# Kernel tuning notes

Hardware: AMD Instinct MI355X
Metric: run time of the kernel (lower is better)

Reference implementation:

```python
import jax, jax.numpy as jnp
import numpy as np

B, S = 2, 2048
HQ, HKV, D = 32, 8, 128
SCALING = 0.08838834764831845  # 1/sqrt(128)
E4M3_MAX = 448.0
FP4_MAX = 6.0
# e2m1 representable magnitudes and decision midpoints
FP4_GRID = jnp.array([0.0, 0.5, 1.0, 1.5, 2.0, 3.0, 4.0, 6.0], dtype=jnp.float32)
FP4_MID = (FP4_GRID[:-1] + FP4_GRID[1:]) / 2.0


def quant_dequant_e4m3(x):
    """Simulate torch .to(float8_e4m3fn): clamp to +-448, round mantissa to 3 bits."""
    ax = jnp.abs(x)
    xc = jnp.clip(x, -E4M3_MAX, E4M3_MAX)
    e = jnp.clip(jnp.floor(jnp.log2(jnp.maximum(ax, 1e-12))), -6.0, 8.0)
    q = jnp.round(xc * jnp.exp2(3.0 - e)) * jnp.exp2(e - 3.0)
    return jnp.where(ax == 0.0, 0.0, q)


def quant_dequant_fp4(x):
    """FP4 (e2m1) compress/decompress with per-(token,head) absmax scale over head_dim.
    x: [B, S, H, D] -> dequantized [B, S, H, D]."""
    scale = jnp.max(jnp.abs(x), axis=-1, keepdims=True) / FP4_MAX  # [B,S,H,1]
    scale = jnp.maximum(scale, 1e-12)
    xn = x / scale
    idx = jnp.searchsorted(FP4_MID, jnp.abs(xn))  # nearest e2m1 magnitude
    return jnp.sign(xn) * FP4_GRID[idx] * scale


def setup_inputs() -> dict:
    key = jax.random.key(0)
    kq, kk, kv = jax.random.split(key, 3)
    q = jax.random.normal(kq, (B, S, HQ * D), dtype=jnp.float32)
    k = jax.random.normal(kk, (B, S, HKV * D), dtype=jnp.float32)
    v = jax.random.normal(kv, (B, S, HKV * D), dtype=jnp.float32)
    return {"q": q, "k": k, "v": v}


def reference(q, k, v):
    # reshape to heads
    qh = q.reshape(B, S, HQ, D)
    kh = k.reshape(B, S, HKV, D)
    vh = v.reshape(B, S, HKV, D)
    # FP8 cast then FP4 compress/decompress of the KV cache
    kq8 = quant_dequant_e4m3(kh)
    vq8 = quant_dequant_e4m3(vh)
    kd = quant_dequant_fp4(kq8)
    vd = quant_dequant_fp4(vq8)
    # GQA: expand kv heads to query heads
    g = HQ // HKV
    kr = jnp.repeat(kd, g, axis=2)  # [B,S,HQ,D]
    vr = jnp.repeat(vd, g, axis=2)
    scores = jnp.einsum("bqhd,bkhd->bhqk", qh, kr) * SCALING  # [B,HQ,S,S]
    causal = jnp.tril(jnp.ones((S, S), dtype=bool))
    scores = jnp.where(causal[None, None], scores, jnp.float32(-1e30))
    probs = jax.nn.softmax(scores, axis=-1)
    out = jnp.einsum("bhqk,bkhd->bqhd", probs, vr)
    return out.reshape(B, S, HQ * D)
```

## Files before the change

### kernel.cpp

```cpp
#include <hip/hip_runtime.h>
#include <cstdint>
#include <cstddef>

#define B_    2
#define S_    2048
#define HQ_   32
#define HKV_  8
#define D_    128
#define SCALING_ 0.08838834764831845f

#define NROW_ (B_*S_*HKV_)

typedef __bf16 bf16x8 __attribute__((ext_vector_type(8)));
typedef float  f32x4  __attribute__((ext_vector_type(4)));

__device__ __forceinline__ unsigned short f2bfu(float f) {
    __bf16 b = (__bf16)f;
    return __builtin_bit_cast(unsigned short, b);
}

__device__ __forceinline__ float qd_e4m3(float x) {
    float ax = fabsf(x);
    float xc = fminf(fmaxf(x, -448.f), 448.f);
    int ex;
    (void)frexpf(fmaxf(ax, 1e-12f), &ex);
    int e = ex - 1;
    e = min(max(e, -6), 8);
    float q = rintf(ldexpf(xc, 3 - e));
    q = ldexpf(q, e - 3);
    return ax == 0.f ? 0.f : q;
}

__device__ __forceinline__ float qd_fp4(float x, float scale) {
    float xn = x / scale;
    float a = fabsf(xn);
    float g;
    if      (a <= 0.25f) g = 0.f;
    else if (a <= 0.75f) g = 0.5f;
    else if (a <= 1.25f) g = 1.f;
    else if (a <= 1.75f) g = 1.5f;
    else if (a <= 2.5f)  g = 2.f;
    else if (a <= 3.5f)  g = 3.f;
    else if (a <= 5.f)   g = 4.f;
    else                 g = 6.f;
    return copysignf(g * scale, xn);
}

__global__ __launch_bounds__(256) void quant_kv(const float* __restrict__ k,
                                                const float* __restrict__ v,
                                                unsigned short* __restrict__ kd,
                                                unsigned short* __restrict__ vd) {
    int gw = (blockIdx.x * 256 + threadIdx.x) >> 6;
    int lane = threadIdx.x & 63;
    int row = gw;
    const float* src;
    unsigned short* dst;
    if (row < NROW_) { src = k; dst = kd; }
    else             { row -= NROW_; src = v; dst = vd; }
    int b   = row / (S_ * HKV_);
    int rem = row - b * (S_ * HKV_);
    int s   = rem >> 3;
    int h   = rem & 7;
    float2 x = *(const float2*)(src + (size_t)row * D_ + 2 * lane);
    float q0 = qd_e4m3(x.x);
    float q1 = qd_e4m3(x.y);
    float amax = fmaxf(fabsf(q0), fabsf(q1));
#pragma unroll
    for (int m = 1; m < 64; m <<= 1) amax = fmaxf(amax, __shfl_xor(amax, m, 64));
    float scale = fmaxf(amax / 6.0f, 1e-12f);
    float y0 = qd_fp4(q0, scale);
    float y1 = qd_fp4(q1, scale);
    size_t outOff = ((size_t)(b * HKV_ + h) * S_ + s) * D_ + 2 * lane;
    unsigned int pack = (unsigned int)f2bfu(y0) | ((unsigned int)f2bfu(y1) << 16);
    *(unsigned int*)(dst + outOff) = pack;
}

__global__ __launch_bounds__(256) void transpose_v(const unsigned short* __restrict__ vd,
                                                   unsigned short* __restrict__ vdT) {
    __shared__ alignas(16) unsigned short t[64][136];
    int bh = blockIdx.x >> 5;
    int st = blockIdx.x & 31;
    int s0 = st * 64;
    int tid = threadIdx.x;
    {
        int row = tid >> 2;
        const unsigned short* sp = vd + ((size_t)bh * S_ + s0 + row) * D_;
#pragma unroll
        for (int i = 0; i < 4; ++i) {
            int c = (tid & 3) + 4 * i;
            *(uint4*)&t[row][c * 8] = *(const uint4*)(sp + c * 8);
        }
    }
    __syncthreads();
    {
        int d = tid >> 1;
        unsigned short* dp = vdT + ((size_t)bh * D_ + d) * S_ + s0;
#pragma unroll
        for (int i = 0; i < 4; ++i) {
            int c = (tid & 1) + 2 * i;
            int so = c * 8;
            unsigned short tmp[8];
#pragma unroll
            for (int e = 0; e < 8; ++e) tmp[e] = t[so + e][d];
            *(uint4*)(dp + so) = *(uint4*)tmp;
        }
    }
}

__global__ __launch_bounds__(256) void attn(const float* __restrict__ q,
                                            const unsigned short* __restrict__ kd,
                                            const unsigned short* __restrict__ vdT,
                                            float* __restrict__ out) {
    int bh = blockIdx.x;
    int yp = blockIdx.y;
    int b  = bh >> 5;
    int hq = bh & 31;
    int hkv = hq >> 2;
    int tid  = threadIdx.x;
    int lane = tid & 63;
    int wave = tid >> 6;
    int m16  = lane & 15;
    int g    = lane >> 4;

    __shared__ alignas(16) unsigned short ks[64 * 128];
    __shared__ alignas(16) unsigned short vs[128 * 64];
    __shared__ alignas(16) unsigned short ps[4 * 16 * 64];

    const unsigned short* kbase = kd  + (size_t)(b * HKV_ + hkv) * S_ * D_;
    const unsigned short* vbase = vdT + (size_t)(b * HKV_ + hkv) * D_ * S_;

    bf16x8 vones;
#pragma unroll
    for (int j = 0; j < 8; ++j) vones[j] = (__bf16)1.0f;

    for (int phase = 0; phase < 2; ++phase) {
        int qt = phase ? yp : (31 - yp);
        int q0 = qt * 64;
        int qrowBase = q0 + wave * 16;

        bf16x8 qf[4];
        const float* qp = q + (((size_t)b * S_ + (qrowBase + m16)) * HQ_ + hq) * D_;
#pragma unroll
        for (int c = 0; c < 4; ++c) {
            const float* p0 = qp + c * 32 + g * 8;
            bf16x8 f;
#pragma unroll
            for (int j = 0; j < 8; ++j) f[j] = (__bf16)(p0[j] * SCALING_);
            qf[c] = f;
        }

        f32x4 o[8];
#pragma unroll
        for (int i = 0; i < 8; ++i) o[i] = (f32x4){0.f, 0.f, 0.f, 0.f};
        f32x4 o9 = (f32x4){0.f, 0.f, 0.f, 0.f};
        float mr[4];
#pragma unroll
        for (int r = 0; r < 4; ++r) mr[r] = -1e30f;

        for (int kt = 0; kt <= qt; ++kt) {
            int k0 = kt * 64;
            __syncthreads();
            {
                int row = tid >> 2;
                const unsigned short* sp = kbase + (size_t)(k0 + row) * D_;
#pragma unroll
                for (int i = 0; i < 4; ++i) {
                    int c = (tid & 3) + 4 * i;
                    *(uint4*)&ks[row * 128 + ((c ^ (row & 15)) * 8)] =
                        *(const uint4*)(sp + c * 8);
                }
            }
            {
                int d = tid >> 1;
                const unsigned short* sp = vbase + (size_t)d * S_ + k0;
#pragma unroll
                for (int i = 0; i < 4; ++i) {
                    int c = (tid & 1) + 2 * i;
                    *(uint4*)&vs[d * 64 + ((c ^ (d & 7)) * 8)] =
                        *(const uint4*)(sp + c * 8);
                }
            }
            __syncthreads();

            f32x4 sacc[4];
#pragma unroll
            for (int n = 0; n < 4; ++n) sacc[n] = (f32x4){0.f, 0.f, 0.f, 0.f};
#pragma unroll
            for (int n = 0; n < 4; ++n) {
#pragma unroll
                for (int c = 0; c < 4; ++c) {
                    bf16x8 bk = *(const bf16x8*)&ks[(n * 16 + m16) * 128 +
                                                    (((c * 4 + g) ^ m16) * 8)];
                    sacc[n] = __builtin_amdgcn_mfma_f32_16x16x32_bf16(qf[c], bk, sacc[n], 0, 0, 0);
                }
            }

            bool diag = (kt == qt);
            float pvv[4][4];
            float rm[4];
#pragma unroll
            for (int r = 0; r < 4; ++r) rm[r] = -1e30f;
#pragma unroll
            for (int n = 0; n < 4; ++n) {
#pragma unroll
                for (int r = 0; r < 4; ++r) {
                    float sc = sacc[n][r];
                    if (diag) {
                        int key = k0 + n * 16 + m16;
                        int qr  = qrowBase + g * 4 + r;
                        if (key > qr) sc = -1e30f;
                    }
                    pvv[n][r] = sc;
                    rm[r] = fmaxf(rm[r], sc);
                }
            }
#pragma unroll
            for (int r = 0; r < 4; ++r) {
#pragma unroll
                for (int mk = 1; mk < 16; mk <<= 1)
                    rm[r] = fmaxf(rm[r], __shfl_xor(rm[r], mk, 64));
                float mnew  = fmaxf(mr[r], rm[r]);
                float alpha = __expf(mr[r] - mnew);
                mr[r] = mnew;
#pragma unroll
                for (int n = 0; n < 4; ++n)
                    pvv[n][r] = __expf(pvv[n][r] - mnew);
#pragma unroll
                for (int ds = 0; ds < 8; ++ds) o[ds][r] *= alpha;
                o9[r] *= alpha;
            }

#pragma unroll
            for (int n = 0; n < 4; ++n)
#pragma unroll
                for (int r = 0; r < 4; ++r) {
                    int prow = g * 4 + r;
                    ps[wave * 1024 + prow * 64 +
                       (((n * 2 + (m16 >> 3)) ^ (prow & 7)) * 8) + (m16 & 7)] =
                        f2bfu(pvv[n][r]);
                }
            asm volatile("s_waitcnt lgkmcnt(0)" ::: "memory");

            bf16x8 pa[2];
#pragma unroll
            for (int kc = 0; kc < 2; ++kc)
                pa[kc] = *(const bf16x8*)&ps[wave * 1024 + m16 * 64 +
                                             (((kc * 4 + g) ^ (m16 & 7)) * 8)];
#pragma unroll
            for (int kc = 0; kc < 2; ++kc)
                o9 = __builtin_amdgcn_mfma_f32_16x16x32_bf16(pa[kc], vones, o9, 0, 0, 0);
#pragma unroll
            for (int ds = 0; ds < 8; ++ds) {
#pragma unroll
                for (int kc = 0; kc < 2; ++kc) {
                    bf16x8 vb = *(const bf16x8*)&vs[(ds * 16 + m16) * 64 +
                                                    (((kc * 4 + g) ^ (m16 & 7)) * 8)];
                    o[ds] = __builtin_amdgcn_mfma_f32_16x16x32_bf16(pa[kc], vb, o[ds], 0, 0, 0);
                }
            }
        }

#pragma unroll
        for (int r = 0; r < 4; ++r) {
            float inv = 1.f / o9[r];
            float* op = out + (((size_t)b * S_ + (qrowBase + g * 4 + r)) * HQ_ + hq) * D_;
#pragma unroll
            for (int ds = 0; ds < 8; ++ds)
                op[ds * 16 + m16] = o[ds][r] * inv;
        }
    }
}

extern "C" void kernel_launch(void* const* d_in, const int* in_sizes, int n_in,
                              void* d_out, int out_size, void* d_ws, size_t ws_size,
                              hipStream_t stream) {
    const float* q = (const float*)d_in[0];
    const float* k = (const float*)d_in[1];
    const float* v = (const float*)d_in[2];
    float* out = (float*)d_out;

    unsigned short* kd  = (unsigned short*)d_ws;
    unsigned short* vd  = kd + (size_t)NROW_ * D_;
    unsigned short* vdT = vd + (size_t)NROW_ * D_;

    quant_kv<<<16384, 256, 0, stream>>>(k, v, kd, vd);
    transpose_v<<<512, 256, 0, stream>>>(vd, vdT);
    attn<<<dim3(64, 16), 256, 0, stream>>>(q, kd, vdT, out);
}
```

Before: 304.0 us.

## Transpose score MFMA, skip masked diagonal tiles, async LDS loads, exp2 softmax

```diff
diff --git a/kernel.cpp b/kernel.cpp
--- a/kernel.cpp
+++ b/kernel.cpp
@@ -8,6 +8,7 @@
 #define HKV_  8
 #define D_    128
 #define SCALING_ 0.08838834764831845f
+#define QSCALE_ (0.08838834764831845f * 1.4426950408889634f)
 
 #define NROW_ (B_*S_*HKV_)
 
@@ -19,15 +20,21 @@
     return __builtin_bit_cast(unsigned short, b);
 }
 
+__device__ __forceinline__ void gl_lds16(const unsigned short* g, unsigned short* l) {
+    __builtin_amdgcn_global_load_lds(
+        (const __attribute__((address_space(1))) void*)g,
+        (__attribute__((address_space(3))) void*)l, 16, 0, 0);
+}
+
 __device__ __forceinline__ float qd_e4m3(float x) {
     float ax = fabsf(x);
     float xc = fminf(fmaxf(x, -448.f), 448.f);
-    int ex;
-    (void)frexpf(fmaxf(ax, 1e-12f), &ex);
-    int e = ex - 1;
+    float axc = fmaxf(ax, 1e-12f);
+    int e = (int)((__builtin_bit_cast(unsigned int, axc) >> 23) & 255u) - 127;
     e = min(max(e, -6), 8);
-    float q = rintf(ldexpf(xc, 3 - e));
-    q = ldexpf(q, e - 3);
+    float s1 = __builtin_bit_cast(float, (unsigned int)(130 - e) << 23);
+    float s2 = __builtin_bit_cast(float, (unsigned int)(124 + e) << 23);
+    float q = rintf(xc * s1) * s2;
     return ax == 0.f ? 0.f : q;
 }
 
@@ -121,6 +128,7 @@
     int wave = tid >> 6;
     int m16  = lane & 15;
     int g    = lane >> 4;
+    int m8   = m16 & 7;
 
     __shared__ alignas(16) unsigned short ks[64 * 128];
     __shared__ alignas(16) unsigned short vs[128 * 64];
@@ -128,10 +136,6 @@
 
     const unsigned short* kbase = kd  + (size_t)(b * HKV_ + hkv) * S_ * D_;
     const unsigned short* vbase = vdT + (size_t)(b * HKV_ + hkv) * D_ * S_;
-
-    bf16x8 vones;
-#pragma unroll
-    for (int j = 0; j < 8; ++j) vones[j] = (__bf16)1.0f;
 
     for (int phase = 0; phase < 2; ++phase) {
         int qt = phase ? yp : (31 - yp);
@@ -145,124 +149,136 @@
             const float* p0 = qp + c * 32 + g * 8;
             bf16x8 f;
 #pragma unroll
-            for (int j = 0; j < 8; ++j) f[j] = (__bf16)(p0[j] * SCALING_);
+            for (int j = 0; j < 8; ++j) f[j] = (__bf16)(p0[j] * QSCALE_);
             qf[c] = f;
         }
 
         f32x4 o[8];
 #pragma unroll
         for (int i = 0; i < 8; ++i) o[i] = (f32x4){0.f, 0.f, 0.f, 0.f};
-        f32x4 o9 = (f32x4){0.f, 0.f, 0.f, 0.f};
-        float mr[4];
-#pragma unroll
-        for (int r = 0; r < 4; ++r) mr[r] = -1e30f;
+        float mr = -1e30f;
+        float lsum = 0.f;
 
         for (int kt = 0; kt <= qt; ++kt) {
             int k0 = kt * 64;
             __syncthreads();
-            {
-                int row = tid >> 2;
-                const unsigned short* sp = kbase + (size_t)(k0 + row) * D_;
-#pragma unroll
-                for (int i = 0; i < 4; ++i) {
-                    int c = (tid & 3) + 4 * i;
-                    *(uint4*)&ks[row * 128 + ((c ^ (row & 15)) * 8)] =
-                        *(const uint4*)(sp + c * 8);
-                }
-            }
-            {
-                int d = tid >> 1;
-                const unsigned short* sp = vbase + (size_t)d * S_ + k0;
-#pragma unroll
-                for (int i = 0; i < 4; ++i) {
-                    int c = (tid & 1) + 2 * i;
-                    *(uint4*)&vs[d * 64 + ((c ^ (d & 7)) * 8)] =
-                        *(const uint4*)(sp + c * 8);
-                }
+#pragma unroll
+            for (int i = 0; i < 4; ++i) {
+                int row = wave * 16 + i * 4 + (lane >> 4);
+                int c = (lane & 15) ^ (row & 15);
+                gl_lds16(kbase + (size_t)(k0 + row) * D_ + c * 8,
+                         &ks[wave * 2048 + i * 512]);
+            }
+#pragma unroll
+            for (int i = 0; i < 4; ++i) {
+                int d = wave * 32 + i * 8 + (lane >> 3);
+                int c = (lane & 7) ^ (d & 7);
+                gl_lds16(vbase + (size_t)d * S_ + k0 + c * 8,
+                         &vs[wave * 2048 + i * 512]);
             }
             __syncthreads();
 
+            bool diag = (kt == qt);
+            int kcmax = diag ? ((wave >> 1) + 1) : 2;
+
             f32x4 sacc[4];
 #pragma unroll
             for (int n = 0; n < 4; ++n) sacc[n] = (f32x4){0.f, 0.f, 0.f, 0.f};
 #pragma unroll
             for (int n = 0; n < 4; ++n) {
-#pragma unroll
-                for (int c = 0; c < 4; ++c) {
-                    bf16x8 bk = *(const bf16x8*)&ks[(n * 16 + m16) * 128 +
-                                                    (((c * 4 + g) ^ m16) * 8)];
-                    sacc[n] = __builtin_amdgcn_mfma_f32_16x16x32_bf16(qf[c], bk, sacc[n], 0, 0, 0);
-                }
-            }
-
-            bool diag = (kt == qt);
-            float pvv[4][4];
-            float rm[4];
-#pragma unroll
-            for (int r = 0; r < 4; ++r) rm[r] = -1e30f;
+                if (!diag || n <= wave) {
+#pragma unroll
+                    for (int c = 0; c < 4; ++c) {
+                        bf16x8 ak = *(const bf16x8*)&ks[(n * 16 + m16) * 128 +
+                                                        (((c * 4 + g) ^ m16) * 8)];
+                        sacc[n] = __builtin_amdgcn_mfma_f32_16x16x32_bf16(ak, qf[c], sacc[n], 0, 0, 0);
+                    }
+                }
+            }
+
+            int qloc = wave * 16 + m16;
+            float pv[4][4];
+            float rm = -1e30f;
 #pragma unroll
             for (int n = 0; n < 4; ++n) {
-#pragma unroll
-                for (int r = 0; r < 4; ++r) {
-                    float sc = sacc[n][r];
-                    if (diag) {
-                        int key = k0 + n * 16 + m16;
-                        int qr  = qrowBase + g * 4 + r;
-                        if (key > qr) sc = -1e30f;
-                    }
-                    pvv[n][r] = sc;
-                    rm[r] = fmaxf(rm[r], sc);
-                }
-            }
-#pragma unroll
-            for (int r = 0; r < 4; ++r) {
-#pragma unroll
-                for (int mk = 1; mk < 16; mk <<= 1)
-                    rm[r] = fmaxf(rm[r], __shfl_xor(rm[r], mk, 64));
-                float mnew  = fmaxf(mr[r], rm[r]);
-                float alpha = __expf(mr[r] - mnew);
-                mr[r] = mnew;
-#pragma unroll
-                for (int n = 0; n < 4; ++n)
-                    pvv[n][r] = __expf(pvv[n][r] - mnew);
-#pragma unroll
-                for (int ds = 0; ds < 8; ++ds) o[ds][r] *= alpha;
-                o9[r] *= alpha;
-            }
-
-#pragma unroll
-            for (int n = 0; n < 4; ++n)
-#pragma unroll
-                for (int r = 0; r < 4; ++r) {
-                    int prow = g * 4 + r;
-                    ps[wave * 1024 + prow * 64 +
-                       (((n * 2 + (m16 >> 3)) ^ (prow & 7)) * 8) + (m16 & 7)] =
-                        f2bfu(pvv[n][r]);
-                }
+                if (!diag || n <= wave) {
+#pragma unroll
+                    for (int r = 0; r < 4; ++r) {
+                        float sc = sacc[n][r];
+                        if (diag) {
+                            int key = n * 16 + g * 4 + r;
+                            sc = (key <= qloc) ? sc : -1e30f;
+                        }
+                        pv[n][r] = sc;
+                        rm = fmaxf(rm, sc);
+                    }
+                }
+            }
+            rm = fmaxf(rm, __shfl_xor(rm, 16, 64));
+            rm = fmaxf(rm, __shfl_xor(rm, 32, 64));
+            float mnew  = fmaxf(mr, rm);
+            float alpha = exp2f(mr - mnew);
+            mr = mnew;
+            float rs = 0.f;
+#pragma unroll
+            for (int n = 0; n < 4; ++n) {
+                if (!diag || n <= wave) {
+#pragma unroll
+                    for (int r = 0; r < 4; ++r) {
+                        float p = exp2f(pv[n][r] - mnew);
+                        pv[n][r] = p;
+                        rs += p;
+                    }
+                }
+            }
+            rs += __shfl_xor(rs, 16, 64);
+            rs += __shfl_xor(rs, 32, 64);
+            lsum = lsum * alpha + rs;
+
+            float ac[4];
+#pragma unroll
+            for (int r = 0; r < 4; ++r) ac[r] = __shfl(alpha, g * 4 + r, 64);
+#pragma unroll
+            for (int ds = 0; ds < 8; ++ds)
+#pragma unroll
+                for (int r = 0; r < 4; ++r) o[ds][r] *= ac[r];
+
+#pragma unroll
+            for (int n = 0; n < 4; ++n) {
+                if (n < 2 * kcmax) {
+                    unsigned int lo = 0, hi = 0;
+                    if (!diag || n <= wave) {
+                        lo = (unsigned int)f2bfu(pv[n][0]) | ((unsigned int)f2bfu(pv[n][1]) << 16);
+                        hi = (unsigned int)f2bfu(pv[n][2]) | ((unsigned int)f2bfu(pv[n][3]) << 16);
+                    }
+                    int chunk = (n * 2 + (g >> 1)) ^ m8;
+                    uint2 val; val.x = lo; val.y = hi;
+                    *(uint2*)&ps[wave * 1024 + m16 * 64 + chunk * 8 + (g & 1) * 4] = val;
+                }
+            }
             asm volatile("s_waitcnt lgkmcnt(0)" ::: "memory");
 
-            bf16x8 pa[2];
-#pragma unroll
-            for (int kc = 0; kc < 2; ++kc)
-                pa[kc] = *(const bf16x8*)&ps[wave * 1024 + m16 * 64 +
-                                             (((kc * 4 + g) ^ (m16 & 7)) * 8)];
-#pragma unroll
-            for (int kc = 0; kc < 2; ++kc)
-                o9 = __builtin_amdgcn_mfma_f32_16x16x32_bf16(pa[kc], vones, o9, 0, 0, 0);
-#pragma unroll
-            for (int ds = 0; ds < 8; ++ds) {
-#pragma unroll
-                for (int kc = 0; kc < 2; ++kc) {
-                    bf16x8 vb = *(const bf16x8*)&vs[(ds * 16 + m16) * 64 +
-                                                    (((kc * 4 + g) ^ (m16 & 7)) * 8)];
-                    o[ds] = __builtin_amdgcn_mfma_f32_16x16x32_bf16(pa[kc], vb, o[ds], 0, 0, 0);
-                }
-            }
-        }
-
+#pragma unroll
+            for (int kc = 0; kc < 2; ++kc) {
+                if (kc < kcmax) {
+                    bf16x8 pa = *(const bf16x8*)&ps[wave * 1024 + m16 * 64 +
+                                                    (((kc * 4 + g) ^ m8) * 8)];
+#pragma unroll
+                    for (int ds = 0; ds < 8; ++ds) {
+                        bf16x8 vb = *(const bf16x8*)&vs[(ds * 16 + m16) * 64 +
+                                                        (((kc * 4 + g) ^ m8) * 8)];
+                        o[ds] = __builtin_amdgcn_mfma_f32_16x16x32_bf16(pa, vb, o[ds], 0, 0, 0);
+                    }
+                }
+            }
+        }
+
+        float lc[4];
+#pragma unroll
+        for (int r = 0; r < 4; ++r) lc[r] = __shfl(lsum, g * 4 + r, 64);
 #pragma unroll
         for (int r = 0; r < 4; ++r) {
-            float inv = 1.f / o9[r];
+            float inv = 1.f / lc[r];
             float* op = out + (((size_t)b * S_ + (qrowBase + g * 4 + r)) * HQ_ + hq) * D_;
 #pragma unroll
             for (int ds = 0; ds < 8; ++ds)
```

Result: faster. 286.9 us (-5.6%).
